# Performance work log

Measured on AMD Instinct MI355X. Metric: run time of the kernel, lower is better.

The kernel has to match this reference:

```python
import jax, jax.numpy as jnp
import numpy as np

B, K, D = 128, 2048, 512   # batch, out_features (classes), in_features
C = 1.0                    # curvature c


def setup_inputs() -> dict:
    key = jax.random.key(0)
    k1, k2, k3 = jax.random.split(key, 3)
    # inputs must lie strictly inside the Poincare ball of radius 1/sqrt(c)
    v = jax.random.normal(k1, (B, D), jnp.float32)
    inp = v * (0.7 / (1.0 + jnp.linalg.norm(v, axis=-1, keepdims=True)))
    # p is a hyperbolic parameter (init zeros in the module; use small in-ball
    # values here so the math is non-degenerate)
    pv = jax.random.normal(k2, (K, D), jnp.float32)
    p = pv * (0.3 / (1.0 + jnp.linalg.norm(pv, axis=-1, keepdims=True)))
    # a is Euclidean, xavier-uniform scale ~ 1/sqrt(D)
    a = jax.random.normal(k3, (K, D), jnp.float32) * (1.0 / np.sqrt(D))
    return {"inp": inp, "p": p, "a": a}


def hyperbolic_logits(inp, p, a, c):
    """Ganea et al. hyperbolic MLR logits.

    logit_k(x) = (lambda_{p_k} ||a_k|| / sqrt(c))
                 * asinh( 2 sqrt(c) <(-p_k) (+)_c x, a_k>
                          / ((1 - c ||(-p_k)(+)_c x||^2) ||a_k||) )
    """
    c = jnp.float32(c)
    sc = jnp.sqrt(c)
    u = -p                                   # [K,D]
    uv = jnp.einsum('bd,kd->bk', inp, u)     # <u_k, x_b>
    uu = jnp.sum(u * u, -1)                  # [K]
    vv = jnp.sum(inp * inp, -1)              # [B]
    # Mobius addition w = u (+)_c x, broadcast to [B,K,D]
    alpha = 1.0 + 2.0 * c * uv + c * vv[:, None]          # coeff of u
    beta = 1.0 - c * uu[None, :]                           # coeff of x
    den = 1.0 + 2.0 * c * uv + (c * c) * uu[None, :] * vv[:, None]
    w = (alpha[..., None] * u[None, :, :]
         + beta[..., None] * inp[:, None, :]) / den[..., None]   # [B,K,D]
    ww = jnp.sum(w * w, -1)                  # [B,K]
    wa = jnp.einsum('bkd,kd->bk', w, a)      # [B,K]
    a_norm = jnp.linalg.norm(a, axis=-1)     # [K]
    lam_p = 2.0 / (1.0 - c * jnp.sum(p * p, -1))   # conformal factor at p_k
    num = 2.0 * sc * wa
    denom = a_norm[None, :] * (1.0 - c * ww)
    return (lam_p * a_norm / sc)[None, :] * jnp.arcsinh(num / denom)  # [B,K]


def reference(inp, p, a):
    return hyperbolic_logits(inp, p, a, C)
```

## Files before the change

kernel.cpp:

```cpp
#include <hip/hip_runtime.h>
#include <hip/hip_bf16.h>

#define B_SZ 128
#define K_SZ 2048
#define D_SZ 512

typedef __attribute__((ext_vector_type(8))) short short8;
typedef __attribute__((ext_vector_type(4))) float floatx4;


static __device__ inline unsigned short f2b(float f) {
  unsigned int u = __float_as_uint(f);
  return (unsigned short)((u + 0x7fffu + ((u >> 16) & 1u)) >> 16);
}

__global__ __launch_bounds__(256) void prep_kernel(
    const float* __restrict__ x, const float* __restrict__ p,
    const float* __restrict__ a, float* __restrict__ uu,
    float* __restrict__ nua, float* __restrict__ an, float* __restrict__ vv,
    unsigned short* __restrict__ xb, unsigned short* __restrict__ pb,
    unsigned short* __restrict__ ab) {
  int gw = (blockIdx.x * 256 + threadIdx.x) >> 6;
  int lane = threadIdx.x & 63;
  if (gw < K_SZ) {
    const float4* pr = (const float4*)(p + (size_t)gw * D_SZ);
    const float4* ar = (const float4*)(a + (size_t)gw * D_SZ);
    float pp = 0.f, pa = 0.f, aa = 0.f;
#pragma unroll
    for (int i = 0; i < 2; ++i) {
      float4 pv = pr[lane + 64 * i];
      float4 av = ar[lane + 64 * i];
      pp += pv.x * pv.x + pv.y * pv.y + pv.z * pv.z + pv.w * pv.w;
      pa += pv.x * av.x + pv.y * av.y + pv.z * av.z + pv.w * av.w;
      aa += av.x * av.x + av.y * av.y + av.z * av.z + av.w * av.w;
      ushort4 pc, ac;
      pc.x = f2b(pv.x); pc.y = f2b(pv.y); pc.z = f2b(pv.z); pc.w = f2b(pv.w);
      ac.x = f2b(av.x); ac.y = f2b(av.y); ac.z = f2b(av.z); ac.w = f2b(av.w);
      *(ushort4*)(pb + (size_t)gw * D_SZ + (size_t)(lane + 64 * i) * 4) = pc;
      *(ushort4*)(ab + (size_t)gw * D_SZ + (size_t)(lane + 64 * i) * 4) = ac;
    }
#pragma unroll
    for (int off = 32; off > 0; off >>= 1) {
      pp += __shfl_xor(pp, off, 64);
      pa += __shfl_xor(pa, off, 64);
      aa += __shfl_xor(aa, off, 64);
    }
    if (lane == 0) {
      uu[gw] = pp;
      nua[gw] = -pa;
      an[gw] = sqrtf(aa);
    }
  } else if (gw < K_SZ + B_SZ) {
    int b = gw - K_SZ;
    const float4* xr = (const float4*)(x + (size_t)b * D_SZ);
    float s = 0.f;
#pragma unroll
    for (int i = 0; i < 2; ++i) {
      float4 xv = xr[lane + 64 * i];
      s += xv.x * xv.x + xv.y * xv.y + xv.z * xv.z + xv.w * xv.w;
      ushort4 xc;
      xc.x = f2b(xv.x); xc.y = f2b(xv.y); xc.z = f2b(xv.z); xc.w = f2b(xv.w);
      *(ushort4*)(xb + (size_t)b * D_SZ + (size_t)(lane + 64 * i) * 4) = xc;
    }
#pragma unroll
    for (int off = 32; off > 0; off >>= 1) s += __shfl_xor(s, off, 64);
    if (lane == 0) vv[b] = s;
  }
}

__global__ __launch_bounds__(256) void mfma_kernel(
    const unsigned short* __restrict__ xb, const unsigned short* __restrict__ pb,
    const unsigned short* __restrict__ ab, const float* __restrict__ uu,
    const float* __restrict__ nua, const float* __restrict__ an,
    const float* __restrict__ vv, float* __restrict__ out) {
  const int t = threadIdx.x;
  const int wave = t >> 6;
  const int lane = t & 63;
  const int row16 = lane & 15;
  const int quad = lane >> 4;
  const int mt = blockIdx.x & 7;
  const int kg = blockIdx.x >> 3;
  const int kt = kg * 4 + wave;
  const int bm = mt * 16;
  const int kn = kt * 16;

  const short8* arow = (const short8*)(xb + (size_t)(bm + row16) * D_SZ) + quad;
  short8 afrag[16];
#pragma unroll
  for (int dc = 0; dc < 16; ++dc) afrag[dc] = arow[dc * 4];

  const short8* prow = (const short8*)(pb + (size_t)(kn + row16) * D_SZ) + quad;
  const short8* brow = (const short8*)(ab + (size_t)(kn + row16) * D_SZ) + quad;

  floatx4 cs = {0.f, 0.f, 0.f, 0.f};
  floatx4 ca = {0.f, 0.f, 0.f, 0.f};
#pragma unroll
  for (int dc = 0; dc < 16; ++dc) {
    short8 bp = prow[dc * 4];
    short8 bv = brow[dc * 4];
    cs = __builtin_amdgcn_mfma_f32_16x16x32_bf16(afrag[dc], bp, cs, 0, 0, 0);
    ca = __builtin_amdgcn_mfma_f32_16x16x32_bf16(afrag[dc], bv, ca, 0, 0, 0);
  }

  const int k = kn + row16;
  const float uuk = uu[k];
  const float nuak = nua[k];
  const float ank = an[k];
  const float beta = 1.f - uuk;
  const float scale = (2.f / beta) * ank;
#pragma unroll
  for (int r = 0; r < 4; ++r) {
    const int b = bm + quad * 4 + r;
    const float vvb = vv[b];
    const float uv = -cs[r];
    const float xa = ca[r];
    const float alpha = 1.f + 2.f * uv + vvb;
    const float den = 1.f + 2.f * uv + uuk * vvb;
    const float inv = 1.f / den;
    const float ww =
        (alpha * alpha * uuk + 2.f * alpha * beta * uv + beta * beta * vvb) *
        inv * inv;
    const float wa = (alpha * nuak + beta * xa) * inv;
    const float z = 2.f * wa / (ank * (1.f - ww));
    out[(size_t)b * K_SZ + k] = scale * asinhf(z);
  }
}

extern "C" void kernel_launch(void* const* d_in, const int* in_sizes, int n_in,
                              void* d_out, int out_size, void* d_ws, size_t ws_size,
                              hipStream_t stream) {
  const float* x = (const float*)d_in[0];
  const float* p = (const float*)d_in[1];
  const float* a = (const float*)d_in[2];
  float* out = (float*)d_out;

  char* ws = (char*)d_ws;
  float* uu = (float*)(ws + 0);
  float* nua = (float*)(ws + 8192);
  float* an = (float*)(ws + 16384);
  float* vv = (float*)(ws + 24576);
  unsigned short* xb = (unsigned short*)(ws + 25088);
  unsigned short* pb = (unsigned short*)(ws + 156160);
  unsigned short* ab = (unsigned short*)(ws + 2253312);

  prep_kernel<<<(K_SZ + B_SZ) / 4, 256, 0, stream>>>(x, p, a, uu, nua, an, vv,
                                                     xb, pb, ab);
  mfma_kernel<<<(B_SZ / 16) * (K_SZ / 16) / 4, 256, 0, stream>>>(
      xb, pb, ab, uu, nua, an, vv, out);
}
```

Baseline: 72.94 us.

## Split D reduction across waves with LDS reduction, 4x more blocks

Each 16x16 output tile is now handled by a full block whose four waves each take a quarter of the D dimension. Partial MFMA accumulators are combined through shared memory before the per-element epilogue. The grid grows from 256 to 1024 blocks to expose more parallelism and shorten each wave's serial MFMA chain. The cost is an LDS round trip plus a barrier, and the x fragment is now reloaded by every block instead of being reused across four K tiles.

```diff
diff --git a/kernel.cpp b/kernel.cpp
--- a/kernel.cpp
+++ b/kernel.cpp
@@ -68,62 +68,79 @@
   }
 }
 
-__global__ __launch_bounds__(256) void mfma_kernel(
+__global__ __launch_bounds__(256, 4) void mfma_kernel(
     const unsigned short* __restrict__ xb, const unsigned short* __restrict__ pb,
     const unsigned short* __restrict__ ab, const float* __restrict__ uu,
     const float* __restrict__ nua, const float* __restrict__ an,
     const float* __restrict__ vv, float* __restrict__ out) {
+  __shared__ float rs[4 * 256];
+  __shared__ float ra[4 * 256];
   const int t = threadIdx.x;
-  const int wave = t >> 6;
+  const int w = t >> 6;
   const int lane = t & 63;
   const int row16 = lane & 15;
   const int quad = lane >> 4;
-  const int mt = blockIdx.x & 7;
-  const int kg = blockIdx.x >> 3;
-  const int kt = kg * 4 + wave;
+  const int mt = blockIdx.x >> 7;
+  const int kt = blockIdx.x & 127;
   const int bm = mt * 16;
   const int kn = kt * 16;
+  const int d0 = w * 128;
 
-  const short8* arow = (const short8*)(xb + (size_t)(bm + row16) * D_SZ) + quad;
-  short8 afrag[16];
+  const short8* arow =
+      (const short8*)(xb + (size_t)(bm + row16) * D_SZ + d0) + quad;
+  const short8* prow =
+      (const short8*)(pb + (size_t)(kn + row16) * D_SZ + d0) + quad;
+  const short8* brow =
+      (const short8*)(ab + (size_t)(kn + row16) * D_SZ + d0) + quad;
+
+  short8 af[4], bp[4], bv[4];
 #pragma unroll
-  for (int dc = 0; dc < 16; ++dc) afrag[dc] = arow[dc * 4];
-
-  const short8* prow = (const short8*)(pb + (size_t)(kn + row16) * D_SZ) + quad;
-  const short8* brow = (const short8*)(ab + (size_t)(kn + row16) * D_SZ) + quad;
+  for (int dc = 0; dc < 4; ++dc) {
+    af[dc] = arow[dc * 4];
+    bp[dc] = prow[dc * 4];
+    bv[dc] = brow[dc * 4];
+  }
 
   floatx4 cs = {0.f, 0.f, 0.f, 0.f};
   floatx4 ca = {0.f, 0.f, 0.f, 0.f};
 #pragma unroll
-  for (int dc = 0; dc < 16; ++dc) {
-    short8 bp = prow[dc * 4];
-    short8 bv = brow[dc * 4];
-    cs = __builtin_amdgcn_mfma_f32_16x16x32_bf16(afrag[dc], bp, cs, 0, 0, 0);
-    ca = __builtin_amdgcn_mfma_f32_16x16x32_bf16(afrag[dc], bv, ca, 0, 0, 0);
+  for (int dc = 0; dc < 4; ++dc) {
+    cs = __builtin_amdgcn_mfma_f32_16x16x32_bf16(af[dc], bp[dc], cs, 0, 0, 0);
+    ca = __builtin_amdgcn_mfma_f32_16x16x32_bf16(af[dc], bv[dc], ca, 0, 0, 0);
   }
 
-  const int k = kn + row16;
+  *(floatx4*)&rs[t * 4] = cs;
+  *(floatx4*)&ra[t * 4] = ca;
+  __syncthreads();
+
+  const int m = t >> 4;
+  const int n = t & 15;
+  const int src = ((m >> 2) * 16 + n) * 4 + (m & 3);
+  float sdot = 0.f, adot = 0.f;
+#pragma unroll
+  for (int ww_ = 0; ww_ < 4; ++ww_) {
+    sdot += rs[ww_ * 256 + src];
+    adot += ra[ww_ * 256 + src];
+  }
+
+  const int k = kn + n;
+  const int b = bm + m;
   const float uuk = uu[k];
   const float nuak = nua[k];
   const float ank = an[k];
+  const float vvb = vv[b];
   const float beta = 1.f - uuk;
   const float scale = (2.f / beta) * ank;
-#pragma unroll
-  for (int r = 0; r < 4; ++r) {
-    const int b = bm + quad * 4 + r;
-    const float vvb = vv[b];
-    const float uv = -cs[r];
-    const float xa = ca[r];
-    const float alpha = 1.f + 2.f * uv + vvb;
-    const float den = 1.f + 2.f * uv + uuk * vvb;
-    const float inv = 1.f / den;
-    const float ww =
-        (alpha * alpha * uuk + 2.f * alpha * beta * uv + beta * beta * vvb) *
-        inv * inv;
-    const float wa = (alpha * nuak + beta * xa) * inv;
-    const float z = 2.f * wa / (ank * (1.f - ww));
-    out[(size_t)b * K_SZ + k] = scale * asinhf(z);
-  }
+  const float uv = -sdot;
+  const float alpha = 1.f + 2.f * uv + vvb;
+  const float den = 1.f + 2.f * uv + uuk * vvb;
+  const float inv = 1.f / den;
+  const float wwn =
+      (alpha * alpha * uuk + 2.f * alpha * beta * uv + beta * beta * vvb) *
+      inv * inv;
+  const float wa = (alpha * nuak + beta * adot) * inv;
+  const float z = 2.f * wa / (ank * (1.f - wwn));
+  out[(size_t)b * K_SZ + k] = scale * asinhf(z);
 }
 
 extern "C" void kernel_launch(void* const* d_in, const int* in_sizes, int n_in,
@@ -145,6 +162,6 @@
 
   prep_kernel<<<(K_SZ + B_SZ) / 4, 256, 0, stream>>>(x, p, a, uu, nua, an, vv,
                                                      xb, pb, ab);
-  mfma_kernel<<<(B_SZ / 16) * (K_SZ / 16) / 4, 256, 0, stream>>>(
+  mfma_kernel<<<(B_SZ / 16) * (K_SZ / 16), 256, 0, stream>>>(
       xb, pb, ab, uu, nua, an, vv, out);
 }
```

Result: faster. 69.96 us (-4.1%).

## Fuse prep and MFMA kernels into one with LDS staging and split-D reduction

Applied to the files above, without the earlier changes.

Replaces the two-kernel pipeline (bf16 conversion plus norms into workspace, then MFMA) with a single kernel. Each block loads 32 x rows and 16 p/a rows from fp32, converts them to bf16 into padded LDS, and computes the norms locally. Four waves split the D dimension in halves and reduce partial dot products through LDS before the epilogue. This removes one launch and the workspace round trip, at the cost of converting x redundantly in every block and re-reading p/a across the four batch tiles.

```diff
diff --git a/kernel.cpp b/kernel.cpp
--- a/kernel.cpp
+++ b/kernel.cpp
@@ -4,125 +4,136 @@
 #define B_SZ 128
 #define K_SZ 2048
 #define D_SZ 512
+#define ROWP 520
 
 typedef __attribute__((ext_vector_type(8))) short short8;
 typedef __attribute__((ext_vector_type(4))) float floatx4;
-
 
 static __device__ inline unsigned short f2b(float f) {
   unsigned int u = __float_as_uint(f);
   return (unsigned short)((u + 0x7fffu + ((u >> 16) & 1u)) >> 16);
 }
 
-__global__ __launch_bounds__(256) void prep_kernel(
+__global__ __launch_bounds__(256, 2) void fused_kernel(
     const float* __restrict__ x, const float* __restrict__ p,
-    const float* __restrict__ a, float* __restrict__ uu,
-    float* __restrict__ nua, float* __restrict__ an, float* __restrict__ vv,
-    unsigned short* __restrict__ xb, unsigned short* __restrict__ pb,
-    unsigned short* __restrict__ ab) {
-  int gw = (blockIdx.x * 256 + threadIdx.x) >> 6;
-  int lane = threadIdx.x & 63;
-  if (gw < K_SZ) {
-    const float4* pr = (const float4*)(p + (size_t)gw * D_SZ);
-    const float4* ar = (const float4*)(a + (size_t)gw * D_SZ);
+    const float* __restrict__ a, float* __restrict__ out) {
+  __shared__ unsigned short xs[32 * ROWP];
+  __shared__ unsigned short ps[16 * ROWP];
+  __shared__ unsigned short as_[16 * ROWP];
+  __shared__ float stats[32 + 48];
+
+  const int t = threadIdx.x;
+  const int bm = (blockIdx.x >> 7) * 32;
+  const int kn = (blockIdx.x & 127) * 16;
+
+  {
+    const int r = t >> 3, s = t & 7;
+    const float4* src = (const float4*)(x + (size_t)(bm + r) * D_SZ);
+    float vvp = 0.f;
+#pragma unroll
+    for (int i = 0; i < 16; ++i) {
+      float4 v = src[s + i * 8];
+      vvp += v.x * v.x + v.y * v.y + v.z * v.z + v.w * v.w;
+      ushort4 c;
+      c.x = f2b(v.x); c.y = f2b(v.y); c.z = f2b(v.z); c.w = f2b(v.w);
+      *(ushort4*)&xs[r * ROWP + (s + i * 8) * 4] = c;
+    }
+    vvp += __shfl_xor(vvp, 1, 64);
+    vvp += __shfl_xor(vvp, 2, 64);
+    vvp += __shfl_xor(vvp, 4, 64);
+    if (s == 0) stats[r] = vvp;
+  }
+
+  {
+    const int r = t >> 4, s = t & 15;
+    const float4* sp = (const float4*)(p + (size_t)(kn + r) * D_SZ);
+    const float4* sa = (const float4*)(a + (size_t)(kn + r) * D_SZ);
     float pp = 0.f, pa = 0.f, aa = 0.f;
 #pragma unroll
-    for (int i = 0; i < 2; ++i) {
-      float4 pv = pr[lane + 64 * i];
-      float4 av = ar[lane + 64 * i];
+    for (int i = 0; i < 8; ++i) {
+      float4 pv = sp[s + i * 16];
+      float4 av = sa[s + i * 16];
       pp += pv.x * pv.x + pv.y * pv.y + pv.z * pv.z + pv.w * pv.w;
       pa += pv.x * av.x + pv.y * av.y + pv.z * av.z + pv.w * av.w;
       aa += av.x * av.x + av.y * av.y + av.z * av.z + av.w * av.w;
       ushort4 pc, ac;
       pc.x = f2b(pv.x); pc.y = f2b(pv.y); pc.z = f2b(pv.z); pc.w = f2b(pv.w);
       ac.x = f2b(av.x); ac.y = f2b(av.y); ac.z = f2b(av.z); ac.w = f2b(av.w);
-      *(ushort4*)(pb + (size_t)gw * D_SZ + (size_t)(lane + 64 * i) * 4) = pc;
-      *(ushort4*)(ab + (size_t)gw * D_SZ + (size_t)(lane + 64 * i) * 4) = ac;
+      *(ushort4*)&ps[r * ROWP + (s + i * 16) * 4] = pc;
+      *(ushort4*)&as_[r * ROWP + (s + i * 16) * 4] = ac;
     }
-#pragma unroll
-    for (int off = 32; off > 0; off >>= 1) {
-      pp += __shfl_xor(pp, off, 64);
-      pa += __shfl_xor(pa, off, 64);
-      aa += __shfl_xor(aa, off, 64);
+    pp += __shfl_xor(pp, 1, 64);
+    pa += __shfl_xor(pa, 1, 64);
+    aa += __shfl_xor(aa, 1, 64);
+    pp += __shfl_xor(pp, 2, 64);
+    pa += __shfl_xor(pa, 2, 64);
+    aa += __shfl_xor(aa, 2, 64);
+    pp += __shfl_xor(pp, 4, 64);
+    pa += __shfl_xor(pa, 4, 64);
+    aa += __shfl_xor(aa, 4, 64);
+    pp += __shfl_xor(pp, 8, 64);
+    pa += __shfl_xor(pa, 8, 64);
+    aa += __shfl_xor(aa, 8, 64);
+    if (s == 0) {
+      stats[32 + r] = pp;
+      stats[48 + r] = -pa;
+      stats[64 + r] = sqrtf(aa);
     }
-    if (lane == 0) {
-      uu[gw] = pp;
-      nua[gw] = -pa;
-      an[gw] = sqrtf(aa);
-    }
-  } else if (gw < K_SZ + B_SZ) {
-    int b = gw - K_SZ;
-    const float4* xr = (const float4*)(x + (size_t)b * D_SZ);
-    float s = 0.f;
-#pragma unroll
-    for (int i = 0; i < 2; ++i) {
-      float4 xv = xr[lane + 64 * i];
-      s += xv.x * xv.x + xv.y * xv.y + xv.z * xv.z + xv.w * xv.w;
-      ushort4 xc;
-      xc.x = f2b(xv.x); xc.y = f2b(xv.y); xc.z = f2b(xv.z); xc.w = f2b(xv.w);
-      *(ushort4*)(xb + (size_t)b * D_SZ + (size_t)(lane + 64 * i) * 4) = xc;
-    }
-#pragma unroll
-    for (int off = 32; off > 0; off >>= 1) s += __shfl_xor(s, off, 64);
-    if (lane == 0) vv[b] = s;
   }
-}
+  __syncthreads();
 
-__global__ __launch_bounds__(256) void mfma_kernel(
-    const unsigned short* __restrict__ xb, const unsigned short* __restrict__ pb,
-    const unsigned short* __restrict__ ab, const float* __restrict__ uu,
-    const float* __restrict__ nua, const float* __restrict__ an,
-    const float* __restrict__ vv, float* __restrict__ out) {
-  const int t = threadIdx.x;
-  const int wave = t >> 6;
-  const int lane = t & 63;
-  const int row16 = lane & 15;
-  const int quad = lane >> 4;
-  const int mt = blockIdx.x & 7;
-  const int kg = blockIdx.x >> 3;
-  const int kt = kg * 4 + wave;
-  const int bm = mt * 16;
-  const int kn = kt * 16;
-
-  const short8* arow = (const short8*)(xb + (size_t)(bm + row16) * D_SZ) + quad;
-  short8 afrag[16];
-#pragma unroll
-  for (int dc = 0; dc < 16; ++dc) afrag[dc] = arow[dc * 4];
-
-  const short8* prow = (const short8*)(pb + (size_t)(kn + row16) * D_SZ) + quad;
-  const short8* brow = (const short8*)(ab + (size_t)(kn + row16) * D_SZ) + quad;
-
+  const int w = t >> 6, lane = t & 63;
+  const int row16 = lane & 15, quad = lane >> 4;
+  const int wm = w & 1, dh = w >> 1;
+  const unsigned short* xrow = &xs[(wm * 16 + row16) * ROWP + dh * 256 + quad * 8];
+  const unsigned short* prow = &ps[row16 * ROWP + dh * 256 + quad * 8];
+  const unsigned short* arow = &as_[row16 * ROWP + dh * 256 + quad * 8];
   floatx4 cs = {0.f, 0.f, 0.f, 0.f};
   floatx4 ca = {0.f, 0.f, 0.f, 0.f};
 #pragma unroll
-  for (int dc = 0; dc < 16; ++dc) {
-    short8 bp = prow[dc * 4];
-    short8 bv = brow[dc * 4];
-    cs = __builtin_amdgcn_mfma_f32_16x16x32_bf16(afrag[dc], bp, cs, 0, 0, 0);
-    ca = __builtin_amdgcn_mfma_f32_16x16x32_bf16(afrag[dc], bv, ca, 0, 0, 0);
+  for (int dc = 0; dc < 8; ++dc) {
+    short8 af = *(const short8*)(xrow + dc * 32);
+    short8 bp = *(const short8*)(prow + dc * 32);
+    short8 bv = *(const short8*)(arow + dc * 32);
+    cs = __builtin_amdgcn_mfma_f32_16x16x32_bf16(af, bp, cs, 0, 0, 0);
+    ca = __builtin_amdgcn_mfma_f32_16x16x32_bf16(af, bv, ca, 0, 0, 0);
   }
 
-  const int k = kn + row16;
-  const float uuk = uu[k];
-  const float nuak = nua[k];
-  const float ank = an[k];
-  const float beta = 1.f - uuk;
-  const float scale = (2.f / beta) * ank;
+  __syncthreads();
+  float* part_s = (float*)ps;
+  float* part_a = part_s + 1024;
+  *(floatx4*)&part_s[(w * 64 + lane) * 4] = cs;
+  *(floatx4*)&part_a[(w * 64 + lane) * 4] = ca;
+  __syncthreads();
+
 #pragma unroll
-  for (int r = 0; r < 4; ++r) {
-    const int b = bm + quad * 4 + r;
-    const float vvb = vv[b];
-    const float uv = -cs[r];
-    const float xa = ca[r];
+  for (int o = 0; o < 2; ++o) {
+    const int idx = t + o * 256;
+    const int m16 = idx >> 4;
+    const int n = idx & 15;
+    const int wmI = m16 >> 4, mr = m16 & 15;
+    const int lsrc = ((mr >> 2) << 4) | n;
+    const int reg = mr & 3;
+    const float sdot = part_s[(wmI * 64 + lsrc) * 4 + reg] +
+                       part_s[((2 + wmI) * 64 + lsrc) * 4 + reg];
+    const float adot = part_a[(wmI * 64 + lsrc) * 4 + reg] +
+                       part_a[((2 + wmI) * 64 + lsrc) * 4 + reg];
+    const float vvb = stats[m16];
+    const float uuk = stats[32 + n];
+    const float nuak = stats[48 + n];
+    const float ank = stats[64 + n];
+    const float beta = 1.f - uuk;
+    const float scale = (2.f / beta) * ank;
+    const float uv = -sdot;
     const float alpha = 1.f + 2.f * uv + vvb;
     const float den = 1.f + 2.f * uv + uuk * vvb;
     const float inv = 1.f / den;
-    const float ww =
+    const float wwn =
         (alpha * alpha * uuk + 2.f * alpha * beta * uv + beta * beta * vvb) *
         inv * inv;
-    const float wa = (alpha * nuak + beta * xa) * inv;
-    const float z = 2.f * wa / (ank * (1.f - ww));
-    out[(size_t)b * K_SZ + k] = scale * asinhf(z);
+    const float wa = (alpha * nuak + beta * adot) * inv;
+    const float z = 2.f * wa / (ank * (1.f - wwn));
+    out[(size_t)(bm + m16) * K_SZ + (kn + n)] = scale * asinhf(z);
   }
 }
 
@@ -133,18 +144,7 @@
   const float* p = (const float*)d_in[1];
   const float* a = (const float*)d_in[2];
   float* out = (float*)d_out;
+  (void)d_ws; (void)ws_size;
 
-  char* ws = (char*)d_ws;
-  float* uu = (float*)(ws + 0);
-  float* nua = (float*)(ws + 8192);
-  float* an = (float*)(ws + 16384);
-  float* vv = (float*)(ws + 24576);
-  unsigned short* xb = (unsigned short*)(ws + 25088);
-  unsigned short* pb = (unsigned short*)(ws + 156160);
-  unsigned short* ab = (unsigned short*)(ws + 2253312);
-
-  prep_kernel<<<(K_SZ + B_SZ) / 4, 256, 0, stream>>>(x, p, a, uu, nua, an, vv,
-                                                     xb, pb, ab);
-  mfma_kernel<<<(B_SZ / 16) * (K_SZ / 16) / 4, 256, 0, stream>>>(
-      xb, pb, ab, uu, nua, an, vv, out);
+  fused_kernel<<<(B_SZ / 32) * (K_SZ / 16), 256, 0, stream>>>(x, p, a, out);
 }
```

New measurement: 67.03 us. 1.09x faster.
